# Kernel optimization log

Hardware: AMD Instinct MI355X
Metric: run time of the kernel (lower is better)

Reference implementation:

```python
import jax, jax.numpy as jnp
import numpy as np

D_MODEL = 384
D_INNER = 768   # 2 * d_model
D_STATE = 16
DT_RANK = 24    # ceil(d_model/16)
K_CONV = 4
BATCH = 8
SEQ = 2048
EPS = 1e-5


def _layer_norm(x, w, b):
    mu = x.mean(-1, keepdims=True)
    var = ((x - mu) ** 2).mean(-1, keepdims=True)
    return (x - mu) * jax.lax.rsqrt(var + EPS) * w + b


def _silu(x):
    return x * jax.nn.sigmoid(x)


def _mamba_mixer(x, in_proj, conv_w, conv_b, x_proj, dt_w, dt_b, A_log, Dp, out_proj):
    # x: (B, L, d_model)
    xz = x @ in_proj.T                      # (B, L, 2*d_inner)
    xs, z = jnp.split(xz, 2, axis=-1)       # each (B, L, d_inner)
    # causal depthwise conv1d (pad left k-1)
    xc = jnp.transpose(xs, (0, 2, 1))       # (B, d_inner, L)
    xc = jnp.pad(xc, ((0, 0), (0, 0), (K_CONV - 1, 0)))
    xc = jax.lax.conv_general_dilated(
        xc, conv_w, window_strides=(1,), padding='VALID',
        feature_group_count=D_INNER,
        dimension_numbers=('NCH', 'OIH', 'NCH'))
    xs = _silu(jnp.transpose(xc, (0, 2, 1)) + conv_b)   # (B, L, d_inner)
    # input-dependent SSM parameters
    x_dbl = xs @ x_proj.T                    # (B, L, dt_rank + 2*d_state)
    dt, Bm, Cm = jnp.split(x_dbl, [DT_RANK, DT_RANK + D_STATE], axis=-1)
    dt = jax.nn.softplus(dt @ dt_w.T + dt_b)  # (B, L, d_inner)
    A = -jnp.exp(A_log)                       # (d_inner, d_state)

    def step(h, inp):
        dt_t, B_t, C_t, x_t = inp             # (B,d), (B,N), (B,N), (B,d)
        h = jnp.exp(dt_t[:, :, None] * A) * h + (dt_t * x_t)[:, :, None] * B_t[:, None, :]
        y = jnp.einsum('bdn,bn->bd', h, C_t)
        return h, y

    h0 = jnp.zeros((xs.shape[0], D_INNER, D_STATE), xs.dtype)
    inps = (jnp.moveaxis(dt, 1, 0), jnp.moveaxis(Bm, 1, 0),
            jnp.moveaxis(Cm, 1, 0), jnp.moveaxis(xs, 1, 0))
    _, ys = jax.lax.scan(step, h0, inps)      # ys: (L, B, d_inner)
    y = jnp.moveaxis(ys, 0, 1) + xs * Dp      # skip term D*x
    y = y * _silu(z)                          # gated output
    return y @ out_proj.T                     # (B, L, d_model)


def setup_inputs() -> dict:
    key = jax.random.key(0)
    ks = jax.random.split(key, 10)
    s = 0.02
    A_init = jnp.broadcast_to(jnp.log(jnp.arange(1, D_STATE + 1, dtype=jnp.float32)),
                              (2, D_INNER, D_STATE))
    return {
        'x': jax.random.normal(ks[0], (BATCH, SEQ, D_MODEL), jnp.float32),
        'norm_w': jnp.ones((2, D_MODEL), jnp.float32),
        'norm_b': jnp.zeros((2, D_MODEL), jnp.float32),
        'in_proj': jax.random.normal(ks[1], (2, 2 * D_INNER, D_MODEL)) * s,
        'conv_w': jax.random.normal(ks[2], (2, D_INNER, 1, K_CONV)) * 0.2,
        'conv_b': jax.random.normal(ks[3], (2, D_INNER)) * s,
        'x_proj': jax.random.normal(ks[4], (2, DT_RANK + 2 * D_STATE, D_INNER)) * s,
        'dt_w': jax.random.normal(ks[5], (2, D_INNER, DT_RANK)) * s,
        'dt_b': jax.random.normal(ks[6], (2, D_INNER)) * 0.1 - 4.0,
        'A_log': A_init,
        'Dp': jnp.ones((2, D_INNER), jnp.float32),
        'out_proj': jax.random.normal(ks[7], (2, D_MODEL, D_INNER)) * s,
    }


def reference(x, norm_w, norm_b, in_proj, conv_w, conv_b, x_proj, dt_w, dt_b, A_log, Dp, out_proj):
    def blk(i, h):
        return h + _mamba_mixer(_layer_norm(h, norm_w[i], norm_b[i]),
                                in_proj[i], conv_w[i], conv_b[i], x_proj[i],
                                dt_w[i], dt_b[i], A_log[i], Dp[i], out_proj[i])
    h = blk(0, x)                    # forward-direction block
    h = jnp.flip(h, axis=-2)         # reverse sequence
    h = blk(1, h)                    # backward-direction block
    return jnp.flip(h, axis=-2)      # restore order
```

## Files before the change

kernel.cpp:

```cpp
#include <hip/hip_runtime.h>
#include <hip/hip_bf16.h>
#include <cstddef>

#define D_MODEL 384
#define D_INNER 768
#define D_STATE 16
#define DT_RANK 24
#define K_CONV  4
#define BATCH   8
#define SEQ     2048
#define BL      (BATCH * SEQ)
#define NCHUNK  64
#define LCHUNK  (SEQ / NCHUNK)
#define XDBL_LD 64
#define LOG2E   1.44269504088896f

typedef unsigned short ushort_t;
typedef __bf16 bf16x8 __attribute__((ext_vector_type(8)));
typedef float  f32x4  __attribute__((ext_vector_type(4)));
typedef unsigned short u16x8 __attribute__((ext_vector_type(8)));

#define GLOBAL_AS(p) ((const __attribute__((address_space(1))) void*)(p))
#define LDS_AS(p)    ((__attribute__((address_space(3))) void*)(p))

__device__ __forceinline__ ushort_t f32_to_bf16_rne(float v) {
    unsigned int u = __float_as_uint(v);
    return (ushort_t)((u + 0x7FFFu + ((u >> 16) & 1u)) >> 16);
}
__device__ __forceinline__ float bf16_to_f32(ushort_t u) {
    return __uint_as_float(((unsigned int)u) << 16);
}

__device__ __forceinline__ void pow_tree16(float w1, float* pw) {
    float w2 = w1 * w1, w4 = w2 * w2, w8 = w4 * w4;
    pw[0] = w1;        pw[1] = w2;        pw[2] = w2 * w1;   pw[3] = w4;
    pw[4] = w4 * w1;   pw[5] = w4 * w2;   pw[6] = w4 * pw[2]; pw[7] = w8;
    pw[8] = w8 * w1;   pw[9] = w8 * w2;   pw[10] = w8 * pw[2]; pw[11] = w8 * w4;
    pw[12] = w8 * pw[4]; pw[13] = w8 * pw[5]; pw[14] = w8 * pw[6]; pw[15] = w8 * w8;
}

#define N_INP  (2 * 1536 * D_MODEL)
#define N_OUTP (2 * D_MODEL * D_INNER)
#define N_XP   (2 * 64 * D_INNER)
#define N_CW   (2 * K_CONV * D_INNER)
#define N_AL   (2 * D_STATE * D_INNER)
#define N_DW   (2 * DT_RANK * D_INNER)
#define N_PREP (N_INP + N_OUTP + N_XP + N_CW + N_AL + N_DW)

__global__ __launch_bounds__(256) void prep_kernel(
    const float* __restrict__ in_proj, const float* __restrict__ out_proj,
    const float* __restrict__ x_proj, const float* __restrict__ conv_w,
    const float* __restrict__ A_log, const float* __restrict__ dt_w,
    ushort_t* __restrict__ wbf_in, ushort_t* __restrict__ wbf_out,
    ushort_t* __restrict__ xp_bf, float* __restrict__ cwt,
    float* __restrict__ alt, float* __restrict__ dwt)
{
    int i = blockIdx.x * 256 + threadIdx.x;
    if (i < N_INP) {
        wbf_in[i] = f32_to_bf16_rne(in_proj[i]);
        return;
    }
    i -= N_INP;
    if (i < N_OUTP) {
        wbf_out[i] = f32_to_bf16_rne(out_proj[i]);
        return;
    }
    i -= N_OUTP;
    if (i < N_XP) {
        int c   = i % D_INNER;
        int r   = (i / D_INNER) % 64;
        int dir = i / (64 * D_INNER);
        xp_bf[i] = (r < 56)
            ? f32_to_bf16_rne(x_proj[((size_t)dir * 56 + r) * D_INNER + c])
            : (ushort_t)0;
        return;
    }
    i -= N_XP;
    if (i < N_CW) {
        int c = i % D_INNER, k = (i / D_INNER) % K_CONV, dir = i / (K_CONV * D_INNER);
        cwt[i] = conv_w[((size_t)dir * D_INNER + c) * K_CONV + k];
        return;
    }
    i -= N_CW;
    if (i < N_AL) {
        int d = i % D_INNER, n = (i / D_INNER) % D_STATE, dir = i / (D_STATE * D_INNER);
        alt[i] = A_log[((size_t)dir * D_INNER + d) * D_STATE + n];
        return;
    }
    i -= N_AL;
    if (i < N_DW) {
        int d = i % D_INNER, r = (i / D_INNER) % DT_RANK, dir = i / (DT_RANK * D_INNER);
        dwt[i] = dt_w[((size_t)dir * D_INNER + d) * DT_RANK + r];
    }
}

__global__ __launch_bounds__(256) void check_A_kernel(
    const float* __restrict__ A_log, int* __restrict__ flags)
{
    __shared__ int ok[2];
    int tid = threadIdx.x;
    if (tid < 2) ok[tid] = 1;
    __syncthreads();
    for (int dir = 0; dir < 2; dir++) {
        bool good = true;
        for (int j = tid; j < D_INNER * D_STATE; j += 256) {
            int n = j % D_STATE;
            float v = __expf(A_log[(size_t)dir * D_INNER * D_STATE + j]);
            good = good && (fabsf(v - (float)(n + 1)) <= 1e-4f * (float)(n + 1));
        }
        if (!good) atomicAnd(&ok[dir], 0);
    }
    __syncthreads();
    if (tid < 2) flags[tid] = ok[tid];
}

__global__ __launch_bounds__(384) void ln_kernel(
    const float* __restrict__ in, const float* __restrict__ w,
    const float* __restrict__ b, ushort_t* __restrict__ out)
{
    int row = blockIdx.x;
    int tid = threadIdx.x;
    float v = in[(size_t)row * D_MODEL + tid];
    float s = v, sq = v * v;
    #pragma unroll
    for (int o = 32; o; o >>= 1) {
        s  += __shfl_down(s, o);
        sq += __shfl_down(sq, o);
    }
    __shared__ float ss[6], ssq[6];
    __shared__ float mb[2];
    int wid = tid >> 6;
    if ((tid & 63) == 0) { ss[wid] = s; ssq[wid] = sq; }
    __syncthreads();
    if (tid == 0) {
        float S = 0.f, Q = 0.f;
        #pragma unroll
        for (int k = 0; k < 6; k++) { S += ss[k]; Q += ssq[k]; }
        float mu  = S * (1.0f / D_MODEL);
        float var = Q * (1.0f / D_MODEL) - mu * mu;
        mb[0] = mu;
        mb[1] = rsqrtf(var + 1e-5f);
    }
    __syncthreads();
    float r = (v - mb[0]) * mb[1] * w[tid] + b[tid];
    out[(size_t)row * D_MODEL + tid] = f32_to_bf16_rne(r);
}

__global__ __launch_bounds__(256) void gemm_mfma_b16(
    const ushort_t* __restrict__ A, const ushort_t* __restrict__ W,
    ushort_t* __restrict__ C, int N, int K)
{
    __shared__ __bf16 As[128 * 32];
    __shared__ __bf16 Ws[128 * 32];
    int tid  = threadIdx.x;
    int bm = blockIdx.x, bn = blockIdx.y;
    int lane = tid & 63, wave = tid >> 6;
    int wr = wave >> 1, wc = wave & 1;
    int quad = lane >> 4, l16 = lane & 15;
    int ca = ((quad ^ ((l16 >> 1) & 3))) * 8;
    int cbg = ((tid & 3) ^ ((tid >> 3) & 3)) * 8;

    const ushort_t* Ag = A + (size_t)(bm * 128 + (tid >> 2)) * K + cbg;
    const ushort_t* Wg = W + (size_t)(bn * 128 + (tid >> 2)) * K + cbg;

    f32x4 acc[4][4] = {};

    for (int k0 = 0; k0 < K; k0 += 32) {
        __syncthreads();
        __builtin_amdgcn_global_load_lds(GLOBAL_AS(Ag + k0),
                                         LDS_AS(As + tid * 8), 16, 0, 0);
        __builtin_amdgcn_global_load_lds(GLOBAL_AS(Ag + (size_t)64 * K + k0),
                                         LDS_AS(As + 2048 + tid * 8), 16, 0, 0);
        __builtin_amdgcn_global_load_lds(GLOBAL_AS(Wg + k0),
                                         LDS_AS(Ws + tid * 8), 16, 0, 0);
        __builtin_amdgcn_global_load_lds(GLOBAL_AS(Wg + (size_t)64 * K + k0),
                                         LDS_AS(Ws + 2048 + tid * 8), 16, 0, 0);
        __syncthreads();

        bf16x8 af[4], wf[4];
        #pragma unroll
        for (int i = 0; i < 4; i++)
            af[i] = *(const bf16x8*)(As + (wr * 64 + i * 16 + l16) * 32 + ca);
        #pragma unroll
        for (int j = 0; j < 4; j++)
            wf[j] = *(const bf16x8*)(Ws + (wc * 64 + j * 16 + l16) * 32 + ca);
        #pragma unroll
        for (int i = 0; i < 4; i++)
            #pragma unroll
            for (int j = 0; j < 4; j++)
                acc[i][j] = __builtin_amdgcn_mfma_f32_16x16x32_bf16(
                    af[i], wf[j], acc[i][j], 0, 0, 0);
    }

    #pragma unroll
    for (int i = 0; i < 4; i++) {
        #pragma unroll
        for (int r = 0; r < 4; r++) {
            int row = bm * 128 + wr * 64 + i * 16 + quad * 4 + r;
            #pragma unroll
            for (int j = 0; j < 4; j++) {
                int col = bn * 128 + wc * 64 + j * 16 + l16;
                C[(size_t)row * N + col] = f32_to_bf16_rne(acc[i][j][r]);
            }
        }
    }
}

__global__ __launch_bounds__(256) void gemm_mfma_f32(
    const ushort_t* __restrict__ A, const ushort_t* __restrict__ W,
    const float* __restrict__ resid, float* __restrict__ C, int N, int K)
{
    __shared__ __bf16 As[128 * 32];
    __shared__ __bf16 Ws[128 * 32];
    int tid  = threadIdx.x;
    int bm = blockIdx.x, bn = blockIdx.y;
    int lane = tid & 63, wave = tid >> 6;
    int wr = wave >> 1, wc = wave & 1;
    int quad = lane >> 4, l16 = lane & 15;
    int ca = ((quad ^ ((l16 >> 1) & 3))) * 8;
    int cbg = ((tid & 3) ^ ((tid >> 3) & 3)) * 8;

    const ushort_t* Ag = A + (size_t)(bm * 128 + (tid >> 2)) * K + cbg;
    const ushort_t* Wg = W + (size_t)(bn * 128 + (tid >> 2)) * K + cbg;

    f32x4 acc[4][4] = {};

    for (int k0 = 0; k0 < K; k0 += 32) {
        __syncthreads();
        __builtin_amdgcn_global_load_lds(GLOBAL_AS(Ag + k0),
                                         LDS_AS(As + tid * 8), 16, 0, 0);
        __builtin_amdgcn_global_load_lds(GLOBAL_AS(Ag + (size_t)64 * K + k0),
                                         LDS_AS(As + 2048 + tid * 8), 16, 0, 0);
        __builtin_amdgcn_global_load_lds(GLOBAL_AS(Wg + k0),
                                         LDS_AS(Ws + tid * 8), 16, 0, 0);
        __builtin_amdgcn_global_load_lds(GLOBAL_AS(Wg + (size_t)64 * K + k0),
                                         LDS_AS(Ws + 2048 + tid * 8), 16, 0, 0);
        __syncthreads();

        bf16x8 af[4], wf[4];
        #pragma unroll
        for (int i = 0; i < 4; i++)
            af[i] = *(const bf16x8*)(As + (wr * 64 + i * 16 + l16) * 32 + ca);
        #pragma unroll
        for (int j = 0; j < 4; j++)
            wf[j] = *(const bf16x8*)(Ws + (wc * 64 + j * 16 + l16) * 32 + ca);
        #pragma unroll
        for (int i = 0; i < 4; i++)
            #pragma unroll
            for (int j = 0; j < 4; j++)
                acc[i][j] = __builtin_amdgcn_mfma_f32_16x16x32_bf16(
                    af[i], wf[j], acc[i][j], 0, 0, 0);
    }

    #pragma unroll
    for (int i = 0; i < 4; i++) {
        #pragma unroll
        for (int r = 0; r < 4; r++) {
            int row = bm * 128 + wr * 64 + i * 16 + quad * 4 + r;
            #pragma unroll
            for (int j = 0; j < 4; j++) {
                int col = bn * 128 + wc * 64 + j * 16 + l16;
                size_t idx = (size_t)row * N + col;
                C[idx] = acc[i][j][r] + resid[idx];
            }
        }
    }
}

__global__ __launch_bounds__(256) void xdbl_mfma(
    const ushort_t* __restrict__ A, const ushort_t* __restrict__ W,
    float* __restrict__ C)
{
    __shared__ __bf16 As[128 * 32];
    __shared__ __bf16 Ws[64 * 32];
    int tid  = threadIdx.x;
    int bm = blockIdx.x;
    int lane = tid & 63, wave = tid >> 6;
    int quad = lane >> 4, l16 = lane & 15;
    int ca = ((quad ^ ((l16 >> 1) & 3))) * 8;
    int cbg = ((tid & 3) ^ ((tid >> 3) & 3)) * 8;

    const ushort_t* Ag = A + (size_t)(bm * 128 + (tid >> 2)) * D_INNER + cbg;
    const ushort_t* Wg = W + (size_t)(tid >> 2) * D_INNER + cbg;

    f32x4 acc[2][4] = {};

    for (int k0 = 0; k0 < D_INNER; k0 += 32) {
        __syncthreads();
        __builtin_amdgcn_global_load_lds(GLOBAL_AS(Ag + k0),
                                         LDS_AS(As + tid * 8), 16, 0, 0);
        __builtin_amdgcn_global_load_lds(GLOBAL_AS(Ag + (size_t)64 * D_INNER + k0),
                                         LDS_AS(As + 2048 + tid * 8), 16, 0, 0);
        __builtin_amdgcn_global_load_lds(GLOBAL_AS(Wg + k0),
                                         LDS_AS(Ws + tid * 8), 16, 0, 0);
        __syncthreads();

        bf16x8 af[2], wf[4];
        #pragma unroll
        for (int i = 0; i < 2; i++)
            af[i] = *(const bf16x8*)(As + (wave * 32 + i * 16 + l16) * 32 + ca);
        #pragma unroll
        for (int j = 0; j < 4; j++)
            wf[j] = *(const bf16x8*)(Ws + (j * 16 + l16) * 32 + ca);
        #pragma unroll
        for (int i = 0; i < 2; i++)
            #pragma unroll
            for (int j = 0; j < 4; j++)
                acc[i][j] = __builtin_amdgcn_mfma_f32_16x16x32_bf16(
                    af[i], wf[j], acc[i][j], 0, 0, 0);
    }

    #pragma unroll
    for (int i = 0; i < 2; i++) {
        #pragma unroll
        for (int r = 0; r < 4; r++) {
            int row = bm * 128 + wave * 32 + i * 16 + quad * 4 + r;
            #pragma unroll
            for (int j = 0; j < 4; j++) {
                int col = j * 16 + l16;
                C[(size_t)row * XDBL_LD + col] = acc[i][j][r];
            }
        }
    }
}

__global__ __launch_bounds__(256) void dt_kernel(
    const float* __restrict__ xdbl, const float* __restrict__ dwt,
    const float* __restrict__ dtbias, ushort_t* __restrict__ dtb)
{
    int g    = blockIdx.x % 3;
    int row0 = (blockIdx.x / 3) * 16;
    int tid  = threadIdx.x;
    int d    = g * 256 + tid;
    float w[DT_RANK];
    #pragma unroll
    for (int r = 0; r < DT_RANK; r++) w[r] = dwt[r * D_INNER + d];
    float bias = dtbias[d];
    __shared__ float xd[16][DT_RANK];
    if (tid < 16 * DT_RANK) {
        int rr = tid / DT_RANK, cc = tid % DT_RANK;
        xd[rr][cc] = xdbl[(size_t)(row0 + rr) * XDBL_LD + cc];
    }
    __syncthreads();
    #pragma unroll 4
    for (int i = 0; i < 16; i++) {
        float acc = bias;
        #pragma unroll
        for (int r = 0; r < DT_RANK; r++) acc = fmaf(xd[i][r], w[r], acc);
        float sp = acc > 20.f ? acc : __logf(1.f + __expf(acc));
        dtb[(size_t)(row0 + i) * D_INNER + d] = f32_to_bf16_rne(sp);
    }
}

__global__ __launch_bounds__(256) void conv_silu_kernel(
    const ushort_t* __restrict__ xz, const float* __restrict__ cwt,
    const float* __restrict__ cb, ushort_t* __restrict__ xsc, int dir)
{
    int idx8 = blockIdx.x * 256 + threadIdx.x;
    int c8   = (idx8 % 96) * 8;
    int row  = idx8 / 96;
    int l    = row % SEQ;
    int b0   = row - l;

    float acc[8];
    float4 bv0 = *(const float4*)(cb + c8);
    float4 bv1 = *(const float4*)(cb + c8 + 4);
    acc[0] = bv0.x; acc[1] = bv0.y; acc[2] = bv0.z; acc[3] = bv0.w;
    acc[4] = bv1.x; acc[5] = bv1.y; acc[6] = bv1.z; acc[7] = bv1.w;

    #pragma unroll
    for (int k = 0; k < 4; k++) {
        int ls = dir ? (l + k) : (l - 3 + k);
        int wk = dir ? (3 - k) : k;
        bool ok = dir ? (ls < SEQ) : (ls >= 0);
        if (ok) {
            u16x8 v = *(const u16x8*)(xz + (size_t)(b0 + ls) * 1536 + c8);
            float4 w0 = *(const float4*)(cwt + wk * D_INNER + c8);
            float4 w1 = *(const float4*)(cwt + wk * D_INNER + c8 + 4);
            float wv[8] = {w0.x, w0.y, w0.z, w0.w, w1.x, w1.y, w1.z, w1.w};
            #pragma unroll
            for (int j = 0; j < 8; j++)
                acc[j] = fmaf(bf16_to_f32(v[j]), wv[j], acc[j]);
        }
    }
    u16x8 o;
    #pragma unroll
    for (int j = 0; j < 8; j++) {
        float sg = 1.0f / (1.0f + __expf(-acc[j]));
        o[j] = f32_to_bf16_rne(acc[j] * sg);
    }
    *(u16x8*)(xsc + (size_t)row * D_INNER + c8) = o;
}

__global__ __launch_bounds__(256) void scan_pass1(
    const ushort_t* __restrict__ xsc, const ushort_t* __restrict__ dtb,
    const float* __restrict__ xdbl, const float* __restrict__ alt,
    const int* __restrict__ flag,
    ushort_t* __restrict__ hstate, float* __restrict__ sumdt_buf, int dir)
{
    int g = blockIdx.x % 3;
    int c = (blockIdx.x / 3) % NCHUNK;
    int b = blockIdx.x / (3 * NCHUNK);
    int d = g * 256 + threadIdx.x;
    float h[D_STATE] = {};
    float sdt = 0.f;

    int l0 = dir ? (SEQ - 1 - c * LCHUNK) : (c * LCHUNK);
    ptrdiff_t sN = dir ? -(ptrdiff_t)D_INNER : (ptrdiff_t)D_INNER;
    ptrdiff_t sX = dir ? -(ptrdiff_t)XDBL_LD : (ptrdiff_t)XDBL_LD;
    size_t row0 = (size_t)b * SEQ + l0;
    const ushort_t* pdt = dtb + row0 * D_INNER + d;
    const ushort_t* pxs = xsc + row0 * D_INNER + d;
    const float*    pbc = xdbl + row0 * XDBL_LD + DT_RANK;

    if (flag[0]) {
        for (int i = 0; i < LCHUNK; i++) {
            float dtv = bf16_to_f32(*pdt);
            float xv  = bf16_to_f32(*pxs);
            float dtx = dtv * xv;
            sdt += dtv;
            float pw[D_STATE];
            pow_tree16(__builtin_amdgcn_exp2f(-dtv * LOG2E), pw);
            #pragma unroll
            for (int q = 0; q < 4; q++) {
                float4 Bq = *(const float4*)(pbc + 4 * q);
                h[4*q+0] = fmaf(pw[4*q+0], h[4*q+0], dtx * Bq.x);
                h[4*q+1] = fmaf(pw[4*q+1], h[4*q+1], dtx * Bq.y);
                h[4*q+2] = fmaf(pw[4*q+2], h[4*q+2], dtx * Bq.z);
                h[4*q+3] = fmaf(pw[4*q+3], h[4*q+3], dtx * Bq.w);
            }
            pdt += sN; pxs += sN; pbc += sX;
        }
    } else {
        float A2[D_STATE];
        #pragma unroll
        for (int n = 0; n < D_STATE; n++)
            A2[n] = -__expf(alt[n * D_INNER + d]) * LOG2E;
        for (int i = 0; i < LCHUNK; i++) {
            float dtv = bf16_to_f32(*pdt);
            float xv  = bf16_to_f32(*pxs);
            float dtx = dtv * xv;
            sdt += dtv;
            #pragma unroll
            for (int q = 0; q < 4; q++) {
                float4 Bq = *(const float4*)(pbc + 4 * q);
                h[4*q+0] = fmaf(__builtin_amdgcn_exp2f(dtv * A2[4*q+0]), h[4*q+0], dtx * Bq.x);
                h[4*q+1] = fmaf(__builtin_amdgcn_exp2f(dtv * A2[4*q+1]), h[4*q+1], dtx * Bq.y);
                h[4*q+2] = fmaf(__builtin_amdgcn_exp2f(dtv * A2[4*q+2]), h[4*q+2], dtx * Bq.z);
                h[4*q+3] = fmaf(__builtin_amdgcn_exp2f(dtv * A2[4*q+3]), h[4*q+3], dtx * Bq.w);
            }
            pdt += sN; pxs += sN; pbc += sX;
        }
    }
    size_t cidx = (size_t)(b * NCHUNK + c) * D_INNER + d;
    sumdt_buf[cidx] = sdt;
    #pragma unroll
    for (int n = 0; n < D_STATE; n++)
        hstate[cidx * D_STATE + n] = f32_to_bf16_rne(h[n]);
}

__global__ __launch_bounds__(256) void scan_pass2(
    ushort_t* __restrict__ hstate, const float* __restrict__ sumdt_buf,
    const float* __restrict__ alt)
{
    int gid = blockIdx.x * 256 + threadIdx.x;
    int n = gid & 15;
    int d = (gid >> 4) % D_INNER;
    int b = gid / (16 * D_INNER);
    float A2 = -__expf(alt[n * D_INNER + d]) * LOG2E;
    float h = 0.f;
    for (int c = 0; c < NCHUNK; c++) {
        size_t cidx = (size_t)(b * NCHUNK + c) * D_INNER + d;
        float ho = bf16_to_f32(hstate[cidx * D_STATE + n]);
        hstate[cidx * D_STATE + n] = f32_to_bf16_rne(h);
        h = fmaf(__builtin_amdgcn_exp2f(A2 * sumdt_buf[cidx]), h, ho);
    }
}

__global__ __launch_bounds__(256) void scan_pass3(
    const ushort_t* __restrict__ xsc, const ushort_t* __restrict__ dtb,
    const ushort_t* __restrict__ xz, const float* __restrict__ xdbl,
    const float* __restrict__ alt, const float* __restrict__ Dp,
    const int* __restrict__ flag, const ushort_t* __restrict__ hstate,
    ushort_t* __restrict__ y, int dir)
{
    int g = blockIdx.x % 3;
    int c = (blockIdx.x / 3) % NCHUNK;
    int b = blockIdx.x / (3 * NCHUNK);
    int d = g * 256 + threadIdx.x;
    size_t cidx = (size_t)(b * NCHUNK + c) * D_INNER + d;
    float h[D_STATE];
    #pragma unroll
    for (int n = 0; n < D_STATE; n++)
        h[n] = bf16_to_f32(hstate[cidx * D_STATE + n]);
    float Dd = Dp[d];

    int l0 = dir ? (SEQ - 1 - c * LCHUNK) : (c * LCHUNK);
    ptrdiff_t sN = dir ? -(ptrdiff_t)D_INNER : (ptrdiff_t)D_INNER;
    ptrdiff_t sX = dir ? -(ptrdiff_t)XDBL_LD : (ptrdiff_t)XDBL_LD;
    ptrdiff_t sZ = dir ? -(ptrdiff_t)1536 : (ptrdiff_t)1536;
    size_t row0 = (size_t)b * SEQ + l0;
    const ushort_t* pdt = dtb + row0 * D_INNER + d;
    const ushort_t* pxs = xsc + row0 * D_INNER + d;
    const ushort_t* pz  = xz  + row0 * 1536 + D_INNER + d;
    const float*    pbc = xdbl + row0 * XDBL_LD + DT_RANK;
    ushort_t*       py  = y + row0 * D_INNER + d;

    if (flag[0]) {
        for (int i = 0; i < LCHUNK; i++) {
            float dtv = bf16_to_f32(*pdt);
            float xv  = bf16_to_f32(*pxs);
            float zv  = bf16_to_f32(*pz);
            float dtx = dtv * xv;
            float pw[D_STATE];
            pow_tree16(__builtin_amdgcn_exp2f(-dtv * LOG2E), pw);
            float yv0 = 0.f, yv1 = 0.f;
            #pragma unroll
            for (int q = 0; q < 4; q++) {
                float4 Bq = *(const float4*)(pbc + 4 * q);
                float4 Cq = *(const float4*)(pbc + D_STATE + 4 * q);
                h[4*q+0] = fmaf(pw[4*q+0], h[4*q+0], dtx * Bq.x);
                h[4*q+1] = fmaf(pw[4*q+1], h[4*q+1], dtx * Bq.y);
                h[4*q+2] = fmaf(pw[4*q+2], h[4*q+2], dtx * Bq.z);
                h[4*q+3] = fmaf(pw[4*q+3], h[4*q+3], dtx * Bq.w);
                yv0 = fmaf(h[4*q+0], Cq.x, yv0);
                yv1 = fmaf(h[4*q+1], Cq.y, yv1);
                yv0 = fmaf(h[4*q+2], Cq.z, yv0);
                yv1 = fmaf(h[4*q+3], Cq.w, yv1);
            }
            float yv = fmaf(xv, Dd, yv0 + yv1);
            float sg = 1.f / (1.f + __expf(-zv));
            yv *= zv * sg;
            *py = f32_to_bf16_rne(yv);
            pdt += sN; pxs += sN; pz += sZ; pbc += sX; py += sN;
        }
    } else {
        float A2[D_STATE];
        #pragma unroll
        for (int n = 0; n < D_STATE; n++)
            A2[n] = -__expf(alt[n * D_INNER + d]) * LOG2E;
        for (int i = 0; i < LCHUNK; i++) {
            float dtv = bf16_to_f32(*pdt);
            float xv  = bf16_to_f32(*pxs);
            float zv  = bf16_to_f32(*pz);
            float dtx = dtv * xv;
            float yv0 = 0.f, yv1 = 0.f;
            #pragma unroll
            for (int q = 0; q < 4; q++) {
                float4 Bq = *(const float4*)(pbc + 4 * q);
                float4 Cq = *(const float4*)(pbc + D_STATE + 4 * q);
                h[4*q+0] = fmaf(__builtin_amdgcn_exp2f(dtv * A2[4*q+0]), h[4*q+0], dtx * Bq.x);
                h[4*q+1] = fmaf(__builtin_amdgcn_exp2f(dtv * A2[4*q+1]), h[4*q+1], dtx * Bq.y);
                h[4*q+2] = fmaf(__builtin_amdgcn_exp2f(dtv * A2[4*q+2]), h[4*q+2], dtx * Bq.z);
                h[4*q+3] = fmaf(__builtin_amdgcn_exp2f(dtv * A2[4*q+3]), h[4*q+3], dtx * Bq.w);
                yv0 = fmaf(h[4*q+0], Cq.x, yv0);
                yv1 = fmaf(h[4*q+1], Cq.y, yv1);
                yv0 = fmaf(h[4*q+2], Cq.z, yv0);
                yv1 = fmaf(h[4*q+3], Cq.w, yv1);
            }
            float yv = fmaf(xv, Dd, yv0 + yv1);
            float sg = 1.f / (1.f + __expf(-zv));
            yv *= zv * sg;
            *py = f32_to_bf16_rne(yv);
            pdt += sN; pxs += sN; pz += sZ; pbc += sX; py += sN;
        }
    }
}

extern "C" void kernel_launch(void* const* d_in, const int* in_sizes, int n_in,
                              void* d_out, int out_size, void* d_ws, size_t ws_size,
                              hipStream_t stream)
{
    const float* x       = (const float*)d_in[0];
    const float* norm_w  = (const float*)d_in[1];
    const float* norm_b  = (const float*)d_in[2];
    const float* in_proj = (const float*)d_in[3];
    const float* conv_w  = (const float*)d_in[4];
    const float* conv_b  = (const float*)d_in[5];
    const float* x_proj  = (const float*)d_in[6];
    const float* dt_w    = (const float*)d_in[7];
    const float* dt_b    = (const float*)d_in[8];
    const float* A_log   = (const float*)d_in[9];
    const float* Dp      = (const float*)d_in[10];
    const float* out_proj= (const float*)d_in[11];
    float* out = (float*)d_out;

    float* ws   = (float*)d_ws;
    float* reg0 = ws;                ws += (size_t)BL * D_INNER / 2;
    ushort_t* lnb = (ushort_t*)reg0;
    ushort_t* ybf = (ushort_t*)reg0;
    ushort_t* xzb  = (ushort_t*)ws;  ws += (size_t)BL * 1536 / 2;
    ushort_t* xscb = (ushort_t*)ws;  ws += (size_t)BL * D_INNER / 2;
    ushort_t* dtb  = (ushort_t*)ws;  ws += (size_t)BL * D_INNER / 2;
    float* xdbl = ws;                ws += (size_t)BL * XDBL_LD;
    float* sumdt  = ws;              ws += (size_t)BATCH * NCHUNK * D_INNER;
    ushort_t* hstate = (ushort_t*)ws; ws += (size_t)BATCH * NCHUNK * D_INNER * D_STATE / 2;
    ushort_t* wbf_in  = (ushort_t*)ws;  ws += (size_t)N_INP / 2;
    ushort_t* wbf_out = (ushort_t*)ws;  ws += (size_t)N_OUTP / 2;
    ushort_t* xp_bf   = (ushort_t*)ws;  ws += (size_t)N_XP / 2;
    float* cwt = ws;                 ws += (size_t)N_CW;
    float* alt = ws;                 ws += (size_t)N_AL;
    float* dwt = ws;                 ws += (size_t)N_DW;
    int* aflags = (int*)ws;          ws += 2;

    prep_kernel<<<N_PREP / 256, 256, 0, stream>>>(
        in_proj, out_proj, x_proj, conv_w, A_log, dt_w,
        wbf_in, wbf_out, xp_bf, cwt, alt, dwt);
    check_A_kernel<<<1, 256, 0, stream>>>(A_log, aflags);

    for (int i = 0; i < 2; i++) {
        const float* hinp = (i == 0) ? x : out;
        ln_kernel<<<BL, 384, 0, stream>>>(hinp, norm_w + i * D_MODEL,
                                          norm_b + i * D_MODEL, lnb);
        gemm_mfma_b16<<<dim3(BL / 128, 1536 / 128), 256, 0, stream>>>(
            lnb, wbf_in + (size_t)i * 1536 * D_MODEL, xzb, 1536, D_MODEL);
        conv_silu_kernel<<<(BL * 96) / 256, 256, 0, stream>>>(
            xzb, cwt + (size_t)i * K_CONV * D_INNER, conv_b + i * D_INNER,
            xscb, i);
        xdbl_mfma<<<BL / 128, 256, 0, stream>>>(
            xscb, xp_bf + (size_t)i * 64 * D_INNER, xdbl);
        dt_kernel<<<(BL / 16) * 3, 256, 0, stream>>>(
            xdbl, dwt + (size_t)i * DT_RANK * D_INNER, dt_b + i * D_INNER, dtb);
        scan_pass1<<<BATCH * NCHUNK * 3, 256, 0, stream>>>(
            xscb, dtb, xdbl, alt + (size_t)i * D_STATE * D_INNER,
            aflags + i, hstate, sumdt, i);
        scan_pass2<<<(BATCH * D_INNER * D_STATE) / 256, 256, 0, stream>>>(
            hstate, sumdt, alt + (size_t)i * D_STATE * D_INNER);
        scan_pass3<<<BATCH * NCHUNK * 3, 256, 0, stream>>>(
            xscb, dtb, xzb, xdbl, alt + (size_t)i * D_STATE * D_INNER,
            Dp + i * D_INNER, aflags + i, hstate, ybf, i);
        gemm_mfma_f32<<<dim3(BL / 128, D_MODEL / 128), 256, 0, stream>>>(
            ybf, wbf_out + (size_t)i * D_MODEL * D_INNER, hinp, out,
            D_MODEL, D_INNER);
    }
}
```

Baseline: 489.8 us.

## Store dt transposed channel-major and template scan kernels on direction

dt_kernel now writes softplus(dt) in a channel-major layout (d, row), processing 64 rows per block with 8-wide vector stores. The scan passes read four consecutive dt values with one 8-byte load instead of one strided 2-byte load per timestep. The scan kernels are also templated on direction so strides become compile-time constants. The transposed store means each thread writes 16 bytes at a stride of BL, so writes across threads in a wave are less coalesced than before.

```diff
diff --git a/kernel.cpp b/kernel.cpp
--- a/kernel.cpp
+++ b/kernel.cpp
@@ -19,6 +19,7 @@
 typedef __bf16 bf16x8 __attribute__((ext_vector_type(8)));
 typedef float  f32x4  __attribute__((ext_vector_type(4)));
 typedef unsigned short u16x8 __attribute__((ext_vector_type(8)));
+typedef unsigned short u16x4 __attribute__((ext_vector_type(4)));
 
 #define GLOBAL_AS(p) ((const __attribute__((address_space(1))) void*)(p))
 #define LDS_AS(p)    ((__attribute__((address_space(3))) void*)(p))
@@ -326,29 +327,33 @@
 
 __global__ __launch_bounds__(256) void dt_kernel(
     const float* __restrict__ xdbl, const float* __restrict__ dwt,
-    const float* __restrict__ dtbias, ushort_t* __restrict__ dtb)
+    const float* __restrict__ dtbias, ushort_t* __restrict__ dtb_t)
 {
     int g    = blockIdx.x % 3;
-    int row0 = (blockIdx.x / 3) * 16;
+    int row0 = (blockIdx.x / 3) * 64;
     int tid  = threadIdx.x;
     int d    = g * 256 + tid;
     float w[DT_RANK];
     #pragma unroll
     for (int r = 0; r < DT_RANK; r++) w[r] = dwt[r * D_INNER + d];
     float bias = dtbias[d];
-    __shared__ float xd[16][DT_RANK];
-    if (tid < 16 * DT_RANK) {
-        int rr = tid / DT_RANK, cc = tid % DT_RANK;
+    __shared__ float xd[64][DT_RANK];
+    for (int idx = tid; idx < 64 * DT_RANK; idx += 256) {
+        int rr = idx / DT_RANK, cc = idx % DT_RANK;
         xd[rr][cc] = xdbl[(size_t)(row0 + rr) * XDBL_LD + cc];
     }
     __syncthreads();
-    #pragma unroll 4
-    for (int i = 0; i < 16; i++) {
-        float acc = bias;
-        #pragma unroll
-        for (int r = 0; r < DT_RANK; r++) acc = fmaf(xd[i][r], w[r], acc);
-        float sp = acc > 20.f ? acc : __logf(1.f + __expf(acc));
-        dtb[(size_t)(row0 + i) * D_INNER + d] = f32_to_bf16_rne(sp);
+    for (int i0 = 0; i0 < 64; i0 += 8) {
+        u16x8 o;
+        #pragma unroll
+        for (int i = 0; i < 8; i++) {
+            float acc = bias;
+            #pragma unroll
+            for (int r = 0; r < DT_RANK; r++) acc = fmaf(xd[i0 + i][r], w[r], acc);
+            float sp = acc > 20.f ? acc : __logf(1.f + __expf(acc));
+            o[i] = f32_to_bf16_rne(sp);
+        }
+        *(u16x8*)(dtb_t + (size_t)d * BL + row0 + i0) = o;
     }
 }
 
@@ -392,11 +397,12 @@
     *(u16x8*)(xsc + (size_t)row * D_INNER + c8) = o;
 }
 
+template<int DIR>
 __global__ __launch_bounds__(256) void scan_pass1(
-    const ushort_t* __restrict__ xsc, const ushort_t* __restrict__ dtb,
+    const ushort_t* __restrict__ xsc, const ushort_t* __restrict__ dtb_t,
     const float* __restrict__ xdbl, const float* __restrict__ alt,
     const int* __restrict__ flag,
-    ushort_t* __restrict__ hstate, float* __restrict__ sumdt_buf, int dir)
+    ushort_t* __restrict__ hstate, float* __restrict__ sumdt_buf)
 {
     int g = blockIdx.x % 3;
     int c = (blockIdx.x / 3) % NCHUNK;
@@ -405,51 +411,61 @@
     float h[D_STATE] = {};
     float sdt = 0.f;
 
-    int l0 = dir ? (SEQ - 1 - c * LCHUNK) : (c * LCHUNK);
-    ptrdiff_t sN = dir ? -(ptrdiff_t)D_INNER : (ptrdiff_t)D_INNER;
-    ptrdiff_t sX = dir ? -(ptrdiff_t)XDBL_LD : (ptrdiff_t)XDBL_LD;
+    const int l0 = DIR ? (SEQ - 1 - c * LCHUNK) : (c * LCHUNK);
+    constexpr ptrdiff_t sN = DIR ? -(ptrdiff_t)D_INNER : (ptrdiff_t)D_INNER;
+    constexpr ptrdiff_t sX = DIR ? -(ptrdiff_t)XDBL_LD : (ptrdiff_t)XDBL_LD;
     size_t row0 = (size_t)b * SEQ + l0;
-    const ushort_t* pdt = dtb + row0 * D_INNER + d;
     const ushort_t* pxs = xsc + row0 * D_INNER + d;
     const float*    pbc = xdbl + row0 * XDBL_LD + DT_RANK;
+    const ushort_t* pdtv = dtb_t + (size_t)d * BL + row0;
 
     if (flag[0]) {
-        for (int i = 0; i < LCHUNK; i++) {
-            float dtv = bf16_to_f32(*pdt);
-            float xv  = bf16_to_f32(*pxs);
-            float dtx = dtv * xv;
-            sdt += dtv;
-            float pw[D_STATE];
-            pow_tree16(__builtin_amdgcn_exp2f(-dtv * LOG2E), pw);
-            #pragma unroll
-            for (int q = 0; q < 4; q++) {
-                float4 Bq = *(const float4*)(pbc + 4 * q);
-                h[4*q+0] = fmaf(pw[4*q+0], h[4*q+0], dtx * Bq.x);
-                h[4*q+1] = fmaf(pw[4*q+1], h[4*q+1], dtx * Bq.y);
-                h[4*q+2] = fmaf(pw[4*q+2], h[4*q+2], dtx * Bq.z);
-                h[4*q+3] = fmaf(pw[4*q+3], h[4*q+3], dtx * Bq.w);
+        for (int t = 0; t < 8; t++) {
+            u16x4 dt4 = *(const u16x4*)(DIR ? (pdtv - 3 - 4 * t)
+                                            : (pdtv + 4 * t));
+            #pragma unroll
+            for (int k = 0; k < 4; k++) {
+                float dtv = bf16_to_f32(dt4[DIR ? 3 - k : k]);
+                float xv  = bf16_to_f32(*pxs);
+                float dtx = dtv * xv;
+                sdt += dtv;
+                float pw[D_STATE];
+                pow_tree16(__builtin_amdgcn_exp2f(-dtv * LOG2E), pw);
+                #pragma unroll
+                for (int q = 0; q < 4; q++) {
+                    float4 Bq = *(const float4*)(pbc + 4 * q);
+                    h[4*q+0] = fmaf(pw[4*q+0], h[4*q+0], dtx * Bq.x);
+                    h[4*q+1] = fmaf(pw[4*q+1], h[4*q+1], dtx * Bq.y);
+                    h[4*q+2] = fmaf(pw[4*q+2], h[4*q+2], dtx * Bq.z);
+                    h[4*q+3] = fmaf(pw[4*q+3], h[4*q+3], dtx * Bq.w);
+                }
+                pxs += sN; pbc += sX;
             }
-            pdt += sN; pxs += sN; pbc += sX;
         }
     } else {
         float A2[D_STATE];
         #pragma unroll
         for (int n = 0; n < D_STATE; n++)
             A2[n] = -__expf(alt[n * D_INNER + d]) * LOG2E;
-        for (int i = 0; i < LCHUNK; i++) {
-            float dtv = bf16_to_f32(*pdt);
-            float xv  = bf16_to_f32(*pxs);
-            float dtx = dtv * xv;
-            sdt += dtv;
-            #pragma unroll
-            for (int q = 0; q < 4; q++) {
-                float4 Bq = *(const float4*)(pbc + 4 * q);
-                h[4*q+0] = fmaf(__builtin_amdgcn_exp2f(dtv * A2[4*q+0]), h[4*q+0], dtx * Bq.x);
-                h[4*q+1] = fmaf(__builtin_amdgcn_exp2f(dtv * A2[4*q+1]), h[4*q+1], dtx * Bq.y);
-                h[4*q+2] = fmaf(__builtin_amdgcn_exp2f(dtv * A2[4*q+2]), h[4*q+2], dtx * Bq.z);
-                h[4*q+3] = fmaf(__builtin_amdgcn_exp2f(dtv * A2[4*q+3]), h[4*q+3], dtx * Bq.w);
+        for (int t = 0; t < 8; t++) {
+            u16x4 dt4 = *(const u16x4*)(DIR ? (pdtv - 3 - 4 * t)
+                                            : (pdtv + 4 * t));
+            #pragma unroll
+            for (int k = 0; k < 4; k++) {
+                float dtv = bf16_to_f32(dt4[DIR ? 3 - k : k]);
+                float xv  = bf16_to_f32(*pxs);
+                float dtx = dtv * xv;
+                sdt += dtv;
+                #pragma unroll
+                for (int q = 0; q < 4; q++) {
+                    float4 Bq = *(const float4*)(pbc + 4 * q);
+                    h[4*q+0] = fmaf(__builtin_amdgcn_exp2f(dtv * A2[4*q+0]), h[4*q+0], dtx * Bq.x);
+                    h[4*q+1] = fmaf(__builtin_amdgcn_exp2f(dtv * A2[4*q+1]), h[4*q+1], dtx * Bq.y);
+                    h[4*q+2] = fmaf(__builtin_amdgcn_exp2f(dtv * A2[4*q+2]), h[4*q+2], dtx * Bq.z);
+                    h[4*q+3] = fmaf(__builtin_amdgcn_exp2f(dtv * A2[4*q+3]), h[4*q+3], dtx * Bq.w);
+                }
+                pxs += sN; pbc += sX;
             }
-            pdt += sN; pxs += sN; pbc += sX;
         }
     }
     size_t cidx = (size_t)(b * NCHUNK + c) * D_INNER + d;
@@ -477,12 +493,13 @@
     }
 }
 
+template<int DIR>
 __global__ __launch_bounds__(256) void scan_pass3(
-    const ushort_t* __restrict__ xsc, const ushort_t* __restrict__ dtb,
+    const ushort_t* __restrict__ xsc, const ushort_t* __restrict__ dtb_t,
     const ushort_t* __restrict__ xz, const float* __restrict__ xdbl,
     const float* __restrict__ alt, const float* __restrict__ Dp,
     const int* __restrict__ flag, const ushort_t* __restrict__ hstate,
-    ushort_t* __restrict__ y, int dir)
+    ushort_t* __restrict__ y)
 {
     int g = blockIdx.x % 3;
     int c = (blockIdx.x / 3) % NCHUNK;
@@ -495,74 +512,84 @@
         h[n] = bf16_to_f32(hstate[cidx * D_STATE + n]);
     float Dd = Dp[d];
 
-    int l0 = dir ? (SEQ - 1 - c * LCHUNK) : (c * LCHUNK);
-    ptrdiff_t sN = dir ? -(ptrdiff_t)D_INNER : (ptrdiff_t)D_INNER;
-    ptrdiff_t sX = dir ? -(ptrdiff_t)XDBL_LD : (ptrdiff_t)XDBL_LD;
-    ptrdiff_t sZ = dir ? -(ptrdiff_t)1536 : (ptrdiff_t)1536;
+    const int l0 = DIR ? (SEQ - 1 - c * LCHUNK) : (c * LCHUNK);
+    constexpr ptrdiff_t sN = DIR ? -(ptrdiff_t)D_INNER : (ptrdiff_t)D_INNER;
+    constexpr ptrdiff_t sX = DIR ? -(ptrdiff_t)XDBL_LD : (ptrdiff_t)XDBL_LD;
+    constexpr ptrdiff_t sZ = DIR ? -(ptrdiff_t)1536 : (ptrdiff_t)1536;
     size_t row0 = (size_t)b * SEQ + l0;
-    const ushort_t* pdt = dtb + row0 * D_INNER + d;
     const ushort_t* pxs = xsc + row0 * D_INNER + d;
     const ushort_t* pz  = xz  + row0 * 1536 + D_INNER + d;
     const float*    pbc = xdbl + row0 * XDBL_LD + DT_RANK;
     ushort_t*       py  = y + row0 * D_INNER + d;
+    const ushort_t* pdtv = dtb_t + (size_t)d * BL + row0;
 
     if (flag[0]) {
-        for (int i = 0; i < LCHUNK; i++) {
-            float dtv = bf16_to_f32(*pdt);
-            float xv  = bf16_to_f32(*pxs);
-            float zv  = bf16_to_f32(*pz);
-            float dtx = dtv * xv;
-            float pw[D_STATE];
-            pow_tree16(__builtin_amdgcn_exp2f(-dtv * LOG2E), pw);
-            float yv0 = 0.f, yv1 = 0.f;
-            #pragma unroll
-            for (int q = 0; q < 4; q++) {
-                float4 Bq = *(const float4*)(pbc + 4 * q);
-                float4 Cq = *(const float4*)(pbc + D_STATE + 4 * q);
-                h[4*q+0] = fmaf(pw[4*q+0], h[4*q+0], dtx * Bq.x);
-                h[4*q+1] = fmaf(pw[4*q+1], h[4*q+1], dtx * Bq.y);
-                h[4*q+2] = fmaf(pw[4*q+2], h[4*q+2], dtx * Bq.z);
-                h[4*q+3] = fmaf(pw[4*q+3], h[4*q+3], dtx * Bq.w);
-                yv0 = fmaf(h[4*q+0], Cq.x, yv0);
-                yv1 = fmaf(h[4*q+1], Cq.y, yv1);
-                yv0 = fmaf(h[4*q+2], Cq.z, yv0);
-                yv1 = fmaf(h[4*q+3], Cq.w, yv1);
+        for (int t = 0; t < 8; t++) {
+            u16x4 dt4 = *(const u16x4*)(DIR ? (pdtv - 3 - 4 * t)
+                                            : (pdtv + 4 * t));
+            #pragma unroll
+            for (int k = 0; k < 4; k++) {
+                float dtv = bf16_to_f32(dt4[DIR ? 3 - k : k]);
+                float xv  = bf16_to_f32(*pxs);
+                float zv  = bf16_to_f32(*pz);
+                float dtx = dtv * xv;
+                float pw[D_STATE];
+                pow_tree16(__builtin_amdgcn_exp2f(-dtv * LOG2E), pw);
+                float yv0 = 0.f, yv1 = 0.f;
+                #pragma unroll
+                for (int q = 0; q < 4; q++) {
+                    float4 Bq = *(const float4*)(pbc + 4 * q);
+                    float4 Cq = *(const float4*)(pbc + D_STATE + 4 * q);
+                    h[4*q+0] = fmaf(pw[4*q+0], h[4*q+0], dtx * Bq.x);
+                    h[4*q+1] = fmaf(pw[4*q+1], h[4*q+1], dtx * Bq.y);
+                    h[4*q+2] = fmaf(pw[4*q+2], h[4*q+2], dtx * Bq.z);
+                    h[4*q+3] = fmaf(pw[4*q+3], h[4*q+3], dtx * Bq.w);
+                    yv0 = fmaf(h[4*q+0], Cq.x, yv0);
+                    yv1 = fmaf(h[4*q+1], Cq.y, yv1);
+                    yv0 = fmaf(h[4*q+2], Cq.z, yv0);
+                    yv1 = fmaf(h[4*q+3], Cq.w, yv1);
+                }
+                float yv = fmaf(xv, Dd, yv0 + yv1);
+                float sg = 1.f / (1.f + __expf(-zv));
+                yv *= zv * sg;
+                *py = f32_to_bf16_rne(yv);
+                pxs += sN; pz += sZ; pbc += sX; py += sN;
             }
-            float yv = fmaf(xv, Dd, yv0 + yv1);
-            float sg = 1.f / (1.f + __expf(-zv));
-            yv *= zv * sg;
-            *py = f32_to_bf16_rne(yv);
-            pdt += sN; pxs += sN; pz += sZ; pbc += sX; py += sN;
         }
     } else {
         float A2[D_STATE];
         #pragma unroll
         for (int n = 0; n < D_STATE; n++)
             A2[n] = -__expf(alt[n * D_INNER + d]) * LOG2E;
-        for (int i = 0; i < LCHUNK; i++) {
-            float dtv = bf16_to_f32(*pdt);
-            float xv  = bf16_to_f32(*pxs);
-            float zv  = bf16_to_f32(*pz);
-            float dtx = dtv * xv;
-            float yv0 = 0.f, yv1 = 0.f;
-            #pragma unroll
-            for (int q = 0; q < 4; q++) {
-                float4 Bq = *(const float4*)(pbc + 4 * q);
-                float4 Cq = *(const float4*)(pbc + D_STATE + 4 * q);
-                h[4*q+0] = fmaf(__builtin_amdgcn_exp2f(dtv * A2[4*q+0]), h[4*q+0], dtx * Bq.x);
-                h[4*q+1] = fmaf(__builtin_amdgcn_exp2f(dtv * A2[4*q+1]), h[4*q+1], dtx * Bq.y);
-                h[4*q+2] = fmaf(__builtin_amdgcn_exp2f(dtv * A2[4*q+2]), h[4*q+2], dtx * Bq.z);
-                h[4*q+3] = fmaf(__builtin_amdgcn_exp2f(dtv * A2[4*q+3]), h[4*q+3], dtx * Bq.w);
-                yv0 = fmaf(h[4*q+0], Cq.x, yv0);
-                yv1 = fmaf(h[4*q+1], Cq.y, yv1);
-                yv0 = fmaf(h[4*q+2], Cq.z, yv0);
-                yv1 = fmaf(h[4*q+3], Cq.w, yv1);
+        for (int t = 0; t < 8; t++) {
+            u16x4 dt4 = *(const u16x4*)(DIR ? (pdtv - 3 - 4 * t)
+                                            : (pdtv + 4 * t));
+            #pragma unroll
+            for (int k = 0; k < 4; k++) {
+                float dtv = bf16_to_f32(dt4[DIR ? 3 - k : k]);
+                float xv  = bf16_to_f32(*pxs);
+                float zv  = bf16_to_f32(*pz);
+                float dtx = dtv * xv;
+                float yv0 = 0.f, yv1 = 0.f;
+                #pragma unroll
+                for (int q = 0; q < 4; q++) {
+                    float4 Bq = *(const float4*)(pbc + 4 * q);
+                    float4 Cq = *(const float4*)(pbc + D_STATE + 4 * q);
+                    h[4*q+0] = fmaf(__builtin_amdgcn_exp2f(dtv * A2[4*q+0]), h[4*q+0], dtx * Bq.x);
+                    h[4*q+1] = fmaf(__builtin_amdgcn_exp2f(dtv * A2[4*q+1]), h[4*q+1], dtx * Bq.y);
+                    h[4*q+2] = fmaf(__builtin_amdgcn_exp2f(dtv * A2[4*q+2]), h[4*q+2], dtx * Bq.z);
+                    h[4*q+3] = fmaf(__builtin_amdgcn_exp2f(dtv * A2[4*q+3]), h[4*q+3], dtx * Bq.w);
+                    yv0 = fmaf(h[4*q+0], Cq.x, yv0);
+                    yv1 = fmaf(h[4*q+1], Cq.y, yv1);
+                    yv0 = fmaf(h[4*q+2], Cq.z, yv0);
+                    yv1 = fmaf(h[4*q+3], Cq.w, yv1);
+                }
+                float yv = fmaf(xv, Dd, yv0 + yv1);
+                float sg = 1.f / (1.f + __expf(-zv));
+                yv *= zv * sg;
+                *py = f32_to_bf16_rne(yv);
+                pxs += sN; pz += sZ; pbc += sX; py += sN;
             }
-            float yv = fmaf(xv, Dd, yv0 + yv1);
-            float sg = 1.f / (1.f + __expf(-zv));
-            yv *= zv * sg;
-            *py = f32_to_bf16_rne(yv);
-            pdt += sN; pxs += sN; pz += sZ; pbc += sX; py += sN;
         }
     }
 }
@@ -619,16 +646,26 @@
             xscb, i);
         xdbl_mfma<<<BL / 128, 256, 0, stream>>>(
             xscb, xp_bf + (size_t)i * 64 * D_INNER, xdbl);
-        dt_kernel<<<(BL / 16) * 3, 256, 0, stream>>>(
+        dt_kernel<<<(BL / 64) * 3, 256, 0, stream>>>(
             xdbl, dwt + (size_t)i * DT_RANK * D_INNER, dt_b + i * D_INNER, dtb);
-        scan_pass1<<<BATCH * NCHUNK * 3, 256, 0, stream>>>(
-            xscb, dtb, xdbl, alt + (size_t)i * D_STATE * D_INNER,
-            aflags + i, hstate, sumdt, i);
+        if (i == 0) {
+            scan_pass1<0><<<BATCH * NCHUNK * 3, 256, 0, stream>>>(
+                xscb, dtb, xdbl, alt, aflags, hstate, sumdt);
+        } else {
+            scan_pass1<1><<<BATCH * NCHUNK * 3, 256, 0, stream>>>(
+                xscb, dtb, xdbl, alt + (size_t)D_STATE * D_INNER,
+                aflags + 1, hstate, sumdt);
+        }
         scan_pass2<<<(BATCH * D_INNER * D_STATE) / 256, 256, 0, stream>>>(
             hstate, sumdt, alt + (size_t)i * D_STATE * D_INNER);
-        scan_pass3<<<BATCH * NCHUNK * 3, 256, 0, stream>>>(
-            xscb, dtb, xzb, xdbl, alt + (size_t)i * D_STATE * D_INNER,
-            Dp + i * D_INNER, aflags + i, hstate, ybf, i);
+        if (i == 0) {
+            scan_pass3<0><<<BATCH * NCHUNK * 3, 256, 0, stream>>>(
+                xscb, dtb, xzb, xdbl, alt, Dp, aflags, hstate, ybf);
+        } else {
+            scan_pass3<1><<<BATCH * NCHUNK * 3, 256, 0, stream>>>(
+                xscb, dtb, xzb, xdbl, alt + (size_t)D_STATE * D_INNER,
+                Dp + D_INNER, aflags + 1, hstate, ybf);
+        }
         gemm_mfma_f32<<<dim3(BL / 128, D_MODEL / 128), 256, 0, stream>>>(
             ybf, wbf_out + (size_t)i * D_MODEL * D_INNER, hinp, out,
             D_MODEL, D_INNER);
```

New measurement: 542.8 us. +10.8%, slower.
